# Kernel tuning notes

Measured on AMD Instinct MI355X. Metric: run time of the kernel, lower is better.

## Reference

```python
import jax, jax.numpy as jnp
import numpy as np

N = 50000          # num_entities
R = 16             # num_relations
D = 128            # embedding_dim
B = 4              # num_blocks
d = D // B         # block size (32)
E = 800000         # num edges


def setup_inputs() -> dict:
    key = jax.random.key(0)
    ks = jax.random.split(key, 9)
    s = 1.0 / np.sqrt(D)
    return {
        "edge_index": jax.random.randint(ks[0], (2, E), 0, N),
        "edge_type": jax.random.randint(ks[1], (E,), 0, R),
        "node_emb": jax.random.normal(ks[2], (N, D), jnp.float32) * s,
        "W1": jax.random.normal(ks[3], (R, B, d, d), jnp.float32) * s,
        "root1": jax.random.normal(ks[4], (D, D), jnp.float32) * s,
        "bias1": jax.random.normal(ks[5], (D,), jnp.float32) * 0.01,
        "W2": jax.random.normal(ks[6], (R, B, d, d), jnp.float32) * s,
        "root2": jax.random.normal(ks[7], (D, D), jnp.float32) * s,
        "bias2": jax.random.normal(ks[8], (D,), jnp.float32) * 0.01,
    }


def _rgcn_conv(x, src, dst, et, W, root, bias):
    # x: [N, D]; W: [R, B, d, d] block-diagonal per-relation weights.
    n = x.shape[0]
    # Transform every node under every relation (cheaper than gathering
    # per-edge weight blocks): [R, N, B, d] -> [R, N, D]
    allR = jnp.einsum('nbi,rbio->rnbo', x.reshape(n, B, d), W).reshape(R, n, D)
    msg = allR[et, src]                                   # [E, D] gather
    # Per-relation mean normalization 1/c_{i,r} (PyG RGCNConv aggr='mean'
    # applied per relation): count edges per (dst, relation) pair.
    seg = dst * R + et
    cnt = jax.ops.segment_sum(jnp.ones_like(et, x.dtype), seg, num_segments=n * R)
    norm = 1.0 / jnp.maximum(cnt[seg], 1.0)               # [E]
    agg = jax.ops.segment_sum(msg * norm[:, None], dst, num_segments=n)
    return agg + x @ root + bias


def reference(edge_index, edge_type, node_emb, W1, root1, bias1, W2, root2, bias2):
    src, dst = edge_index[0], edge_index[1]
    h = _rgcn_conv(node_emb, src, dst, edge_type, W1, root1, bias1)
    h = jax.nn.relu(h)  # dropout is identity in eval mode
    return _rgcn_conv(h, src, dst, edge_type, W2, root2, bias2)
```

## Files before the change

kernel.cpp:

```cpp
#include <hip/hip_runtime.h>
#include <hip/hip_bf16.h>

#define N_NODES 50000
#define N_REL   16
#define DIM     128
#define NBLK    4
#define BS      32
#define N_EDGES 800000
#define NSEG    (N_NODES * N_REL)
#define SCAN_BLK 1024
#define N_SCAN_BLKS ((NSEG + SCAN_BLK - 1) / SCAN_BLK)
#define NWT     (N_NODES / 16)

typedef __attribute__((ext_vector_type(8))) short s8v;
typedef __attribute__((ext_vector_type(8))) unsigned short u8v;
typedef __attribute__((ext_vector_type(4))) float f4v;

__device__ __forceinline__ float bf2f(unsigned short u) {
    return __uint_as_float(((unsigned int)u) << 16);
}
__device__ __forceinline__ unsigned short f2bfbits(float f) {
    unsigned int u = __float_as_uint(f);
    return (unsigned short)((u + 0x7fffu + ((u >> 16) & 1u)) >> 16);
}

__global__ __launch_bounds__(256) void count_kernel(const int* __restrict__ src,
                                                    const int* __restrict__ dst,
                                                    const int* __restrict__ et,
                                                    int* __restrict__ cnt,
                                                    int* __restrict__ used, int E) {
    int e = blockIdx.x * 256 + threadIdx.x;
    if (e < E) {
        int r = et[e];
        atomicAdd(&cnt[dst[e] * N_REL + r], 1);
        used[r * N_NODES + src[e]] = 1;
    }
}

__global__ __launch_bounds__(256) void scan1j_kernel(const int* __restrict__ cnt,
                                                     const int* __restrict__ used,
                                                     int* __restrict__ off,
                                                     int* __restrict__ cmap,
                                                     int2* __restrict__ bsum, int M) {
    const int t = threadIdx.x;
    const int base = blockIdx.x * SCAN_BLK + t * 4;
    int c[4], u[4];
#pragma unroll
    for (int i = 0; i < 4; ++i) {
        int idx = base + i;
        c[i] = (idx < M) ? cnt[idx] : 0;
        u[i] = (idx < M) ? used[idx] : 0;
    }
    int cs = c[0] + c[1] + c[2] + c[3];
    int us = u[0] + u[1] + u[2] + u[3];
    const int lane = t & 63, wid = t >> 6;
    int cinc = cs, uinc = us;
    for (int d = 1; d < 64; d <<= 1) {
        int a = __shfl_up(cinc, d, 64);
        int b = __shfl_up(uinc, d, 64);
        if (lane >= d) { cinc += a; uinc += b; }
    }
    __shared__ int cw[5], uw[5];
    if (lane == 63) { cw[wid] = cinc; uw[wid] = uinc; }
    __syncthreads();
    if (t == 0) {
        int a = 0, b = 0;
        for (int w = 0; w < 4; ++w) {
            int x = cw[w]; cw[w] = a; a += x;
            int y = uw[w]; uw[w] = b; b += y;
        }
        cw[4] = a; uw[4] = b;
    }
    __syncthreads();
    int cex = cinc - cs + cw[wid];
    int uex = uinc - us + uw[wid];
#pragma unroll
    for (int i = 0; i < 4; ++i) {
        int idx = base + i;
        if (idx < M) { off[idx] = cex; cmap[idx] = uex; }
        cex += c[i]; uex += u[i];
    }
    if (t == 0) bsum[blockIdx.x] = make_int2(cw[4], uw[4]);
}

__global__ __launch_bounds__(1024) void scan2j_kernel(int2* __restrict__ bsum, int nb) {
    const int t = threadIdx.x;
    int2 s = (t < nb) ? bsum[t] : make_int2(0, 0);
    const int lane = t & 63, wid = t >> 6;
    int ci = s.x, ui = s.y;
    for (int d = 1; d < 64; d <<= 1) {
        int a = __shfl_up(ci, d, 64);
        int b = __shfl_up(ui, d, 64);
        if (lane >= d) { ci += a; ui += b; }
    }
    __shared__ int cw[16], uw[16];
    if (lane == 63) { cw[wid] = ci; uw[wid] = ui; }
    __syncthreads();
    if (t == 0) {
        int a = 0, b = 0;
        for (int w = 0; w < 16; ++w) {
            int x = cw[w]; cw[w] = a; a += x;
            int y = uw[w]; uw[w] = b; b += y;
        }
    }
    __syncthreads();
    if (t < nb) bsum[t] = make_int2(ci - s.x + cw[wid], ui - s.y + uw[wid]);
}

__global__ __launch_bounds__(256) void scan3j_kernel(int* __restrict__ off,
                                                     int* __restrict__ cmap,
                                                     const int2* __restrict__ bsum, int M) {
    int i = blockIdx.x * 256 + threadIdx.x;
    if (i < M) {
        int2 b = bsum[i / SCAN_BLK];
        off[i] += b.x;
        cmap[i] += b.y;
    }
}

__global__ __launch_bounds__(256) void scatter_fast_kernel(const int* __restrict__ src,
                                                           const int* __restrict__ dst,
                                                           const int* __restrict__ et,
                                                           int* __restrict__ off,
                                                           const int* __restrict__ cnt,
                                                           const int* __restrict__ cmap,
                                                           int2* __restrict__ evec, int E) {
    int e = blockIdx.x * 256 + threadIdx.x;
    if (e < E) {
        int r = et[e];
        int seg = dst[e] * N_REL + r;
        int pos = atomicAdd(&off[seg], 1);
        float inv = 1.0f / (float)cnt[seg];
        int g = cmap[r * N_NODES + src[e]];
        evec[pos] = make_int2(g, __float_as_int(inv));
    }
}

__global__ __launch_bounds__(256) void scan1_kernel(const int* __restrict__ in,
                                                    int* __restrict__ out,
                                                    int* __restrict__ bsum, int M) {
    const int t = threadIdx.x;
    const int base = blockIdx.x * SCAN_BLK + t * 4;
    int v0 = (base + 0 < M) ? in[base + 0] : 0;
    int v1 = (base + 1 < M) ? in[base + 1] : 0;
    int v2 = (base + 2 < M) ? in[base + 2] : 0;
    int v3 = (base + 3 < M) ? in[base + 3] : 0;
    const int s = v0 + v1 + v2 + v3;
    const int lane = t & 63, wid = t >> 6;
    int inc = s;
    for (int d = 1; d < 64; d <<= 1) {
        int u = __shfl_up(inc, d, 64);
        if (lane >= d) inc += u;
    }
    __shared__ int wsum[5];
    if (lane == 63) wsum[wid] = inc;
    __syncthreads();
    if (t == 0) {
        int a = 0;
        for (int w = 0; w < 4; ++w) { int u = wsum[w]; wsum[w] = a; a += u; }
        wsum[4] = a;
    }
    __syncthreads();
    const int ex = inc - s + wsum[wid];
    if (base + 0 < M) out[base + 0] = ex;
    if (base + 1 < M) out[base + 1] = ex + v0;
    if (base + 2 < M) out[base + 2] = ex + v0 + v1;
    if (base + 3 < M) out[base + 3] = ex + v0 + v1 + v2;
    if (t == 0) bsum[blockIdx.x] = wsum[4];
}

__global__ __launch_bounds__(1024) void scan2_kernel(int* __restrict__ bsum, int nb) {
    const int t = threadIdx.x;
    int s = (t < nb) ? bsum[t] : 0;
    const int lane = t & 63, wid = t >> 6;
    int inc = s;
    for (int d = 1; d < 64; d <<= 1) {
        int u = __shfl_up(inc, d, 64);
        if (lane >= d) inc += u;
    }
    __shared__ int wsum[16];
    if (lane == 63) wsum[wid] = inc;
    __syncthreads();
    if (t == 0) {
        int a = 0;
        for (int w = 0; w < 16; ++w) { int u = wsum[w]; wsum[w] = a; a += u; }
    }
    __syncthreads();
    const int ex = inc - s + wsum[wid];
    if (t < nb) bsum[t] = ex;
}

__global__ __launch_bounds__(256) void scan3_kernel(int* __restrict__ out,
                                                    const int* __restrict__ bsum, int M) {
    int i = blockIdx.x * 256 + threadIdx.x;
    if (i < M) out[i] += bsum[i / SCAN_BLK];
}

__global__ __launch_bounds__(256) void scatter_old_kernel(const int* __restrict__ src,
                                                          const int* __restrict__ dst,
                                                          const int* __restrict__ et,
                                                          int* __restrict__ off,
                                                          int* __restrict__ srcs, int E) {
    int e = blockIdx.x * 256 + threadIdx.x;
    if (e < E) {
        int seg = dst[e] * N_REL + et[e];
        int pos = atomicAdd(&off[seg], 1);
        srcs[pos] = src[e];
    }
}

__global__ __launch_bounds__(256) void prep_kernel(const float* __restrict__ W1,
                                                   const float* __restrict__ W2,
                                                   const float* __restrict__ r1,
                                                   const float* __restrict__ r2,
                                                   ushort* __restrict__ WB1,
                                                   ushort* __restrict__ WB2,
                                                   ushort* __restrict__ RB1,
                                                   ushort* __restrict__ RB2) {
    int t = blockIdx.x * 256 + threadIdx.x;
    if (t < 262144) {
        const float* W = (t < 131072) ? W1 : W2;
        ushort* WB     = (t < 131072) ? WB1 : WB2;
        int idx = t & 131071;
        int i  = idx & 7;
        int lm = (idx >> 3) & 15;
        int kg = (idx >> 7) & 3;
        int mt = (idx >> 9) & 1;
        int b  = (idx >> 10) & 3;
        int r  = idx >> 12;
        WB[idx] = f2bfbits(W[((size_t)(r * 4 + b) * 32 + kg * 8 + i) * 32 + mt * 16 + lm]);
    } else if (t < 294912) {
        int u = t - 262144;
        const float* R = (u < 16384) ? r1 : r2;
        ushort* RB     = (u < 16384) ? RB1 : RB2;
        int idx = u & 16383;
        int i  = idx & 7;
        int lm = (idx >> 3) & 15;
        int kg = (idx >> 7) & 3;
        int kc = (idx >> 9) & 3;
        int mt = (idx >> 11) & 7;
        RB[idx] = f2bfbits(R[(size_t)(kc * 32 + kg * 8 + i) * DIM + mt * 16 + lm]);
    }
}

template<bool IN_BF16, bool OUT_BF16, bool RELU>
__global__ __launch_bounds__(256) void fused_kernel(const void* __restrict__ xin,
                                                    const ushort* __restrict__ WB,
                                                    const ushort* __restrict__ RB,
                                                    const float* __restrict__ bias,
                                                    const int* __restrict__ used,
                                                    const int* __restrict__ cmap,
                                                    char* __restrict__ tab,
                                                    float* __restrict__ scl,
                                                    void* __restrict__ outv) {
    const int wv = threadIdx.x >> 6;
    const int l  = threadIdx.x & 63;
    const int wt = blockIdx.x * 4 + wv;
    if (wt >= NWT) return;
    const int lm = l & 15;
    const int kg = l >> 4;
    const int node = wt * 16 + lm;
    const int y = blockIdx.y;

    s8v bfr[4];
#pragma unroll
    for (int b = 0; b < 4; ++b) {
        if (IN_BF16) {
            const ushort* xp = (const ushort*)xin + (size_t)node * DIM + b * BS + kg * 8;
            u8v u = *(const u8v*)xp;
#pragma unroll
            for (int i = 0; i < 8; ++i) {
                unsigned short us = u[i];
                if (RELU) us = (us & 0x8000u) ? (unsigned short)0 : us;
                bfr[b][i] = (short)us;
            }
        } else {
            const float* xp = (const float*)xin + (size_t)node * DIM + b * BS + kg * 8;
#pragma unroll
            for (int i = 0; i < 8; ++i) {
                float v = xp[i];
                if (RELU) v = fmaxf(v, 0.f);
                bfr[b][i] = (short)f2bfbits(v);
            }
        }
    }

    if (y < 4) {
        const int rbase = y * 4;
#pragma unroll 2
        for (int ri = 0; ri < 4; ++ri) {
            const int rr = rbase + ri;
            const int grow = rr * N_NODES + node;
            const int flag = used[grow];
            const int cid  = cmap[grow];
            f4v acc[4][2];
#pragma unroll
            for (int b = 0; b < 4; ++b) {
#pragma unroll
                for (int mt = 0; mt < 2; ++mt) {
                    s8v afrag = *(const s8v*)&WB[((((rr * 4 + b) * 2 + mt) * 4 + kg) * 16 + lm) * 8];
                    f4v z = {0.f, 0.f, 0.f, 0.f};
                    acc[b][mt] = __builtin_amdgcn_mfma_f32_16x16x32_bf16(afrag, bfr[b], z, 0, 0, 0);
                }
            }
            float t8[8];
#pragma unroll
            for (int b = 0; b < 4; ++b)
#pragma unroll
                for (int mt = 0; mt < 2; ++mt)
                    t8[b * 2 + mt] = fmaxf(fmaxf(fabsf(acc[b][mt][0]), fabsf(acc[b][mt][1])),
                                           fmaxf(fabsf(acc[b][mt][2]), fabsf(acc[b][mt][3])));
            float m = fmaxf(fmaxf(fmaxf(t8[0], t8[1]), fmaxf(t8[2], t8[3])),
                            fmaxf(fmaxf(t8[4], t8[5]), fmaxf(t8[6], t8[7])));
            m = fmaxf(m, __shfl_xor(m, 16, 64));
            m = fmaxf(m, __shfl_xor(m, 32, 64));
            m = fmaxf(m, 1e-30f);

            if (flag) {
                const float qs = 127.0f / m;
                unsigned int d[8];
#pragma unroll
                for (int b = 0; b < 4; ++b) {
#pragma unroll
                    for (int mt = 0; mt < 2; ++mt) {
                        int q0 = __float2int_rn(acc[b][mt][0] * qs);
                        int q1 = __float2int_rn(acc[b][mt][1] * qs);
                        int q2 = __float2int_rn(acc[b][mt][2] * qs);
                        int q3 = __float2int_rn(acc[b][mt][3] * qs);
                        unsigned int t01 = __builtin_amdgcn_perm((unsigned)q1, (unsigned)q0, 0x00000400u);
                        unsigned int t23 = __builtin_amdgcn_perm((unsigned)q3, (unsigned)q2, 0x00000400u);
                        d[b * 2 + mt] = __builtin_amdgcn_perm(t23, t01, 0x05040100u);
                    }
                }
                char* gp = tab + (size_t)cid * 128 + kg * 32;
                *(uint4*)gp        = make_uint4(d[0], d[1], d[2], d[3]);
                *(uint4*)(gp + 16) = make_uint4(d[4], d[5], d[6], d[7]);
                if (kg == 0) scl[cid] = m * (1.0f / 127.0f);
            }
        }
        return;
    }

#pragma unroll 2
    for (int mt = 0; mt < 8; ++mt) {
        const int col0 = mt * 16 + kg * 4;
        f4v acc = *(const f4v*)&bias[col0];
#pragma unroll
        for (int kc = 0; kc < 4; ++kc) {
            s8v afrag = *(const s8v*)&RB[(((mt * 4 + kc) * 4 + kg) * 16 + lm) * 8];
            acc = __builtin_amdgcn_mfma_f32_16x16x32_bf16(afrag, bfr[kc], acc, 0, 0, 0);
        }
        if (OUT_BF16) {
            unsigned int p0 = (unsigned int)f2bfbits(acc[0]) |
                              ((unsigned int)f2bfbits(acc[1]) << 16);
            unsigned int p1 = (unsigned int)f2bfbits(acc[2]) |
                              ((unsigned int)f2bfbits(acc[3]) << 16);
            *(uint2*)((ushort*)outv + (size_t)node * DIM + col0) = make_uint2(p0, p1);
        } else {
            *(f4v*)((float*)outv + (size_t)node * DIM + col0) = acc;
        }
    }
}

template<bool OUT_BF16>
__global__ __launch_bounds__(256) void agg8_kernel(const int2* __restrict__ evec,
                                                   const int* __restrict__ off,
                                                   const char* __restrict__ tab,
                                                   const float* __restrict__ scl,
                                                   void* __restrict__ outv) {
    const int hw = threadIdx.x >> 5;
    const int o  = threadIdx.x & 31;
    const int v  = blockIdx.x * 8 + hw;

    const int start = (v == 0) ? 0 : off[v * N_REL - 1];
    const int end   = off[v * N_REL + N_REL - 1];

    const int p = o >> 4;
    const int w = o & 15;

    float acc[8];
#pragma unroll
    for (int j = 0; j < 8; ++j) acc[j] = 0.f;

#pragma unroll 2
    for (int base = start; base < end; base += 4) {
        const int k0 = base + p;
        const int k1 = base + 2 + p;
        const int2 e0 = evec[min(k0, end - 1)];
        const int2 e1 = evec[min(k1, end - 1)];
        const int g0 = e0.x, g1 = e1.x;
        const float i0 = (k0 < end) ? __int_as_float(e0.y) : 0.f;
        const float i1 = (k1 < end) ? __int_as_float(e1.y) : 0.f;
        const uint2 q0 = *(const uint2*)(tab + (size_t)g0 * 128 + w * 8);
        const uint2 q1 = *(const uint2*)(tab + (size_t)g1 * 128 + w * 8);
        const float s0 = scl[g0] * i0;
        const float s1 = scl[g1] * i1;
#pragma unroll
        for (int j = 0; j < 4; ++j) {
            acc[j]     = fmaf((float)(int)(signed char)(q0.x >> (8 * j)), s0, acc[j]);
            acc[4 + j] = fmaf((float)(int)(signed char)(q0.y >> (8 * j)), s0, acc[4 + j]);
        }
#pragma unroll
        for (int j = 0; j < 4; ++j) {
            acc[j]     = fmaf((float)(int)(signed char)(q1.x >> (8 * j)), s1, acc[j]);
            acc[4 + j] = fmaf((float)(int)(signed char)(q1.y >> (8 * j)), s1, acc[4 + j]);
        }
    }
#pragma unroll
    for (int j = 0; j < 8; ++j)
        acc[j] += __shfl_xor(acc[j], 16, 32);

    if (o < 16) {
        const int base0 = (o & 3) * 32 + (o >> 2) * 4;
        if (OUT_BF16) {
            ushort* hp = (ushort*)outv + (size_t)v * DIM + base0;
            ushort4 a0 = *(ushort4*)hp;
            ushort4 a1 = *(ushort4*)(hp + 16);
            a0.x = f2bfbits(bf2f(a0.x) + acc[0]);
            a0.y = f2bfbits(bf2f(a0.y) + acc[1]);
            a0.z = f2bfbits(bf2f(a0.z) + acc[2]);
            a0.w = f2bfbits(bf2f(a0.w) + acc[3]);
            a1.x = f2bfbits(bf2f(a1.x) + acc[4]);
            a1.y = f2bfbits(bf2f(a1.y) + acc[5]);
            a1.z = f2bfbits(bf2f(a1.z) + acc[6]);
            a1.w = f2bfbits(bf2f(a1.w) + acc[7]);
            *(ushort4*)hp        = a0;
            *(ushort4*)(hp + 16) = a1;
        } else {
            float* op = (float*)outv + (size_t)v * DIM + base0;
            float4 r0 = *(float4*)op;
            float4 r1 = *(float4*)(op + 16);
            r0.x += acc[0]; r0.y += acc[1]; r0.z += acc[2]; r0.w += acc[3];
            r1.x += acc[4]; r1.y += acc[5]; r1.z += acc[6]; r1.w += acc[7];
            *(float4*)op        = r0;
            *(float4*)(op + 16) = r1;
        }
    }
}

template<bool RELU>
__global__ __launch_bounds__(256) void dense_old_kernel(const float* __restrict__ x,
                                                        const float* __restrict__ root,
                                                        const float* __restrict__ bias,
                                                        float* __restrict__ out) {
    const int wv = threadIdx.x >> 6;
    const int l  = threadIdx.x & 63;
    const int wt = blockIdx.x * 4 + wv;
    if (wt >= NWT) return;
    const int nbase = wt * 16;
    const int lm = l & 15;
    const int kg = l >> 4;
    const int node = nbase + lm;

    s8v bfr[4];
#pragma unroll
    for (int kc = 0; kc < 4; ++kc) {
        const float* xp = &x[(size_t)node * DIM + kc * BS + kg * 8];
#pragma unroll
        for (int i = 0; i < 8; ++i) {
            float v = xp[i];
            if (RELU) v = fmaxf(v, 0.f);
            bfr[kc][i] = (short)f2bfbits(v);
        }
    }
#pragma unroll 2
    for (int mt = 0; mt < 8; ++mt) {
        const int col0 = mt * 16 + kg * 4;
        f4v acc = *(const f4v*)&bias[col0];
#pragma unroll
        for (int kc = 0; kc < 4; ++kc) {
            const float* rp = &root[(size_t)(kc * BS + kg * 8) * DIM + mt * 16 + lm];
            s8v afrag;
#pragma unroll
            for (int i = 0; i < 8; ++i)
                afrag[i] = (short)f2bfbits(rp[i * DIM]);
            acc = __builtin_amdgcn_mfma_f32_16x16x32_bf16(afrag, bfr[kc], acc, 0, 0, 0);
        }
        *(f4v*)&out[(size_t)node * DIM + col0] = acc;
    }
}

template<bool RELU>
__global__ __launch_bounds__(256) void agg_fallback_kernel(const int* __restrict__ srcs,
                                                           const int* __restrict__ off,
                                                           const int* __restrict__ cnt,
                                                           const float* __restrict__ x,
                                                           const float* __restrict__ W,
                                                           float* __restrict__ out) {
    __shared__ float Wsh[N_REL * BS * BS];
    const int bblk = blockIdx.y;
    for (int idx = threadIdx.x * 4; idx < N_REL * BS * BS; idx += 1024) {
        int r = idx >> 10, rest = idx & 1023;
        *(float4*)&Wsh[idx] = *(const float4*)&W[(r * NBLK + bblk) * 1024 + rest];
    }
    __syncthreads();
    const int hw = threadIdx.x >> 5;
    const int o  = threadIdx.x & 31;
    const int v  = blockIdx.x * 8 + hw;
    int endv = 0, cv = 0;
    if (o < N_REL) { endv = off[v * N_REL + o]; cv = cnt[v * N_REL + o]; }
    float acc = out[v * DIM + bblk * BS + o];
    for (int r = 0; r < N_REL; ++r) {
        const int c = __shfl(cv, r, 32);
        if (c == 0) continue;
        const int end = __shfl(endv, r, 32);
        float xs = 0.f;
        for (int k = end - c; k < end; ++k) {
            const int s = srcs[k];
            float xv = x[s * DIM + bblk * BS + o];
            if (RELU) xv = fmaxf(xv, 0.f);
            xs += xv;
        }
        xs *= (1.0f / (float)c);
        const float* wr = &Wsh[r * (BS * BS)];
#pragma unroll
        for (int i = 0; i < BS; i += 2) {
            float xi0 = __shfl(xs, i, 32);
            float xi1 = __shfl(xs, i + 1, 32);
            acc = fmaf(xi0, wr[i * BS + o], acc);
            acc = fmaf(xi1, wr[(i + 1) * BS + o], acc);
        }
    }
    out[v * DIM + bblk * BS + o] = acc;
}

extern "C" void kernel_launch(void* const* d_in, const int* in_sizes, int n_in,
                              void* d_out, int out_size, void* d_ws, size_t ws_size,
                              hipStream_t stream) {
    const int*   edge_index = (const int*)d_in[0];
    const int*   src   = edge_index;
    const int*   dstv  = edge_index + N_EDGES;
    const int*   et    = (const int*)d_in[1];
    const float* x0    = (const float*)d_in[2];
    const float* W1    = (const float*)d_in[3];
    const float* root1 = (const float*)d_in[4];
    const float* bias1 = (const float*)d_in[5];
    const float* W2    = (const float*)d_in[6];
    const float* root2 = (const float*)d_in[7];
    const float* bias2 = (const float*)d_in[8];
    float* out = (float*)d_out;

    char* ws = (char*)d_ws;
    ushort* h    = (ushort*)ws;
    int*    cnt  = (int*)   (ws + 12800000);
    int*    used = (int*)   (ws + 16000000);
    int*    off  = (int*)   (ws + 19200000);
    int*    cmap = (int*)   (ws + 22400000);
    int2*   evec = (int2*)  (ws + 25600000);
    int2*   bsum = (int2*)  (ws + 32000000);
    ushort* WB1  = (ushort*)(ws + 32008192);
    ushort* WB2  = (ushort*)(ws + 32270336);
    ushort* RB1  = (ushort*)(ws + 32532480);
    ushort* RB2  = (ushort*)(ws + 32565248);
    float*  scl  = (float*) (ws + 32598016);
    char*   tab  =          (ws + 35798016);
    const size_t FAST_NEED = 138198016ull;

    const int egrid = (N_EDGES + 255) / 256;
    const int tgrid = (NWT + 3) / 4;

    if (ws_size >= FAST_NEED) {
        prep_kernel<<<1152, 256, 0, stream>>>(W1, W2, root1, root2, WB1, WB2, RB1, RB2);
        hipMemsetAsync(cnt, 0, 2 * (size_t)NSEG * sizeof(int), stream);
        count_kernel<<<egrid, 256, 0, stream>>>(src, dstv, et, cnt, used, N_EDGES);
        scan1j_kernel<<<N_SCAN_BLKS, 256, 0, stream>>>(cnt, used, off, cmap, bsum, NSEG);
        scan2j_kernel<<<1, 1024, 0, stream>>>(bsum, N_SCAN_BLKS);
        scan3j_kernel<<<(NSEG + 255) / 256, 256, 0, stream>>>(off, cmap, bsum, NSEG);
        scatter_fast_kernel<<<egrid, 256, 0, stream>>>(src, dstv, et, off, cnt, cmap,
                                                       evec, N_EDGES);

        dim3 fgrid(tgrid, 5);
        const int ngrid = N_NODES / 8;

        fused_kernel<false, true, false><<<fgrid, 256, 0, stream>>>(
            x0, WB1, RB1, bias1, used, cmap, tab, scl, h);
        agg8_kernel<true><<<ngrid, 256, 0, stream>>>(evec, off, tab, scl, h);

        fused_kernel<true, false, true><<<fgrid, 256, 0, stream>>>(
            h, WB2, RB2, bias2, used, cmap, tab, scl, out);
        agg8_kernel<false><<<ngrid, 256, 0, stream>>>(evec, off, tab, scl, out);
    } else {
        float* hf    = (float*)d_ws;
        int*   cntf  = (int*)((char*)d_ws + 25600000);
        int*   offf  = (int*)((char*)d_ws + 28800000);
        int*   srcsf = (int*)((char*)d_ws + 32000000);
        int*   bsumf = (int*)((char*)d_ws + 35200000);
        int*   usedD = offf;

        hipMemsetAsync(cntf, 0, (size_t)NSEG * sizeof(int), stream);
        count_kernel<<<egrid, 256, 0, stream>>>(src, dstv, et, cntf, usedD, N_EDGES);
        scan1_kernel<<<N_SCAN_BLKS, 256, 0, stream>>>(cntf, offf, bsumf, NSEG);
        scan2_kernel<<<1, 1024, 0, stream>>>(bsumf, N_SCAN_BLKS);
        scan3_kernel<<<(NSEG + 255) / 256, 256, 0, stream>>>(offf, bsumf, NSEG);
        scatter_old_kernel<<<egrid, 256, 0, stream>>>(src, dstv, et, offf, srcsf, N_EDGES);

        dim3 fgrid2(N_NODES / 8, NBLK);
        dense_old_kernel<false><<<tgrid, 256, 0, stream>>>(x0, root1, bias1, hf);
        agg_fallback_kernel<false><<<fgrid2, 256, 0, stream>>>(srcsf, offf, cntf, x0, W1, hf);
        dense_old_kernel<true><<<tgrid, 256, 0, stream>>>(hf, root2, bias2, out);
        agg_fallback_kernel<true><<<fgrid2, 256, 0, stream>>>(srcsf, offf, cntf, hf, W2, out);
    }
}
```

Measured before the change: 255.7 us.

## Fold scan block offsets into consumers and regroup fused kernel relations

Drops the third scan pass that added per-block prefix sums into the offset and compaction arrays. Each consumer (scatter, fused transform, aggregation) now adds the block sum itself when it reads. Separately, the fused kernel grid shrinks from 5 y-slices to 2: each slice handles 8 relations, and slice 0 also computes the root/bias dense part. This saves one kernel launch and a full pass over 800k entries, at the cost of extra bsum loads and less parallelism in the fused kernel.

After: 244.6 us. 1.05x faster.

```diff
diff --git a/kernel.cpp b/kernel.cpp
--- a/kernel.cpp
+++ b/kernel.cpp
@@ -107,31 +107,22 @@
     if (t < nb) bsum[t] = make_int2(ci - s.x + cw[wid], ui - s.y + uw[wid]);
 }
 
-__global__ __launch_bounds__(256) void scan3j_kernel(int* __restrict__ off,
-                                                     int* __restrict__ cmap,
-                                                     const int2* __restrict__ bsum, int M) {
-    int i = blockIdx.x * 256 + threadIdx.x;
-    if (i < M) {
-        int2 b = bsum[i / SCAN_BLK];
-        off[i] += b.x;
-        cmap[i] += b.y;
-    }
-}
-
 __global__ __launch_bounds__(256) void scatter_fast_kernel(const int* __restrict__ src,
                                                            const int* __restrict__ dst,
                                                            const int* __restrict__ et,
                                                            int* __restrict__ off,
                                                            const int* __restrict__ cnt,
                                                            const int* __restrict__ cmap,
+                                                           const int2* __restrict__ bsum,
                                                            int2* __restrict__ evec, int E) {
     int e = blockIdx.x * 256 + threadIdx.x;
     if (e < E) {
         int r = et[e];
         int seg = dst[e] * N_REL + r;
-        int pos = atomicAdd(&off[seg], 1);
+        int pos = atomicAdd(&off[seg], 1) + bsum[seg >> 10].x;
         float inv = 1.0f / (float)cnt[seg];
-        int g = cmap[r * N_NODES + src[e]];
+        int grow = r * N_NODES + src[e];
+        int g = cmap[grow] + bsum[grow >> 10].y;
         evec[pos] = make_int2(g, __float_as_int(inv));
     }
 }
@@ -250,6 +241,7 @@
                                                     const float* __restrict__ bias,
                                                     const int* __restrict__ used,
                                                     const int* __restrict__ cmap,
+                                                    const int2* __restrict__ bsum,
                                                     char* __restrict__ tab,
                                                     float* __restrict__ scl,
                                                     void* __restrict__ outv) {
@@ -257,10 +249,10 @@
     const int l  = threadIdx.x & 63;
     const int wt = blockIdx.x * 4 + wv;
     if (wt >= NWT) return;
+    const int rbase = blockIdx.y * 8;
     const int lm = l & 15;
     const int kg = l >> 4;
     const int node = wt * 16 + lm;
-    const int y = blockIdx.y;
 
     s8v bfr[4];
 #pragma unroll
@@ -285,79 +277,77 @@
         }
     }
 
-    if (y < 4) {
-        const int rbase = y * 4;
 #pragma unroll 2
-        for (int ri = 0; ri < 4; ++ri) {
-            const int rr = rbase + ri;
-            const int grow = rr * N_NODES + node;
-            const int flag = used[grow];
-            const int cid  = cmap[grow];
-            f4v acc[4][2];
+    for (int ri = 0; ri < 8; ++ri) {
+        const int rr = rbase + ri;
+        const int grow = rr * N_NODES + node;
+        const int flag = used[grow];
+        const int cid  = cmap[grow] + bsum[grow >> 10].y;
+        f4v acc[4][2];
+#pragma unroll
+        for (int b = 0; b < 4; ++b) {
+#pragma unroll
+            for (int mt = 0; mt < 2; ++mt) {
+                s8v afrag = *(const s8v*)&WB[((((rr * 4 + b) * 2 + mt) * 4 + kg) * 16 + lm) * 8];
+                f4v z = {0.f, 0.f, 0.f, 0.f};
+                acc[b][mt] = __builtin_amdgcn_mfma_f32_16x16x32_bf16(afrag, bfr[b], z, 0, 0, 0);
+            }
+        }
+        float t8[8];
+#pragma unroll
+        for (int b = 0; b < 4; ++b)
+#pragma unroll
+            for (int mt = 0; mt < 2; ++mt)
+                t8[b * 2 + mt] = fmaxf(fmaxf(fabsf(acc[b][mt][0]), fabsf(acc[b][mt][1])),
+                                       fmaxf(fabsf(acc[b][mt][2]), fabsf(acc[b][mt][3])));
+        float m = fmaxf(fmaxf(fmaxf(t8[0], t8[1]), fmaxf(t8[2], t8[3])),
+                        fmaxf(fmaxf(t8[4], t8[5]), fmaxf(t8[6], t8[7])));
+        m = fmaxf(m, __shfl_xor(m, 16, 64));
+        m = fmaxf(m, __shfl_xor(m, 32, 64));
+        m = fmaxf(m, 1e-30f);
+
+        if (flag) {
+            const float qs = 127.0f / m;
+            unsigned int d[8];
 #pragma unroll
             for (int b = 0; b < 4; ++b) {
 #pragma unroll
                 for (int mt = 0; mt < 2; ++mt) {
-                    s8v afrag = *(const s8v*)&WB[((((rr * 4 + b) * 2 + mt) * 4 + kg) * 16 + lm) * 8];
-                    f4v z = {0.f, 0.f, 0.f, 0.f};
-                    acc[b][mt] = __builtin_amdgcn_mfma_f32_16x16x32_bf16(afrag, bfr[b], z, 0, 0, 0);
+                    int q0 = __float2int_rn(acc[b][mt][0] * qs);
+                    int q1 = __float2int_rn(acc[b][mt][1] * qs);
+                    int q2 = __float2int_rn(acc[b][mt][2] * qs);
+                    int q3 = __float2int_rn(acc[b][mt][3] * qs);
+                    unsigned int t01 = __builtin_amdgcn_perm((unsigned)q1, (unsigned)q0, 0x00000400u);
+                    unsigned int t23 = __builtin_amdgcn_perm((unsigned)q3, (unsigned)q2, 0x00000400u);
+                    d[b * 2 + mt] = __builtin_amdgcn_perm(t23, t01, 0x05040100u);
                 }
             }
-            float t8[8];
-#pragma unroll
-            for (int b = 0; b < 4; ++b)
-#pragma unroll
-                for (int mt = 0; mt < 2; ++mt)
-                    t8[b * 2 + mt] = fmaxf(fmaxf(fabsf(acc[b][mt][0]), fabsf(acc[b][mt][1])),
-                                           fmaxf(fabsf(acc[b][mt][2]), fabsf(acc[b][mt][3])));
-            float m = fmaxf(fmaxf(fmaxf(t8[0], t8[1]), fmaxf(t8[2], t8[3])),
-                            fmaxf(fmaxf(t8[4], t8[5]), fmaxf(t8[6], t8[7])));
-            m = fmaxf(m, __shfl_xor(m, 16, 64));
-            m = fmaxf(m, __shfl_xor(m, 32, 64));
-            m = fmaxf(m, 1e-30f);
-
-            if (flag) {
-                const float qs = 127.0f / m;
-                unsigned int d[8];
-#pragma unroll
-                for (int b = 0; b < 4; ++b) {
-#pragma unroll
-                    for (int mt = 0; mt < 2; ++mt) {
-                        int q0 = __float2int_rn(acc[b][mt][0] * qs);
-                        int q1 = __float2int_rn(acc[b][mt][1] * qs);
-                        int q2 = __float2int_rn(acc[b][mt][2] * qs);
-                        int q3 = __float2int_rn(acc[b][mt][3] * qs);
-                        unsigned int t01 = __builtin_amdgcn_perm((unsigned)q1, (unsigned)q0, 0x00000400u);
-                        unsigned int t23 = __builtin_amdgcn_perm((unsigned)q3, (unsigned)q2, 0x00000400u);
-                        d[b * 2 + mt] = __builtin_amdgcn_perm(t23, t01, 0x05040100u);
-                    }
-                }
-                char* gp = tab + (size_t)cid * 128 + kg * 32;
-                *(uint4*)gp        = make_uint4(d[0], d[1], d[2], d[3]);
-                *(uint4*)(gp + 16) = make_uint4(d[4], d[5], d[6], d[7]);
-                if (kg == 0) scl[cid] = m * (1.0f / 127.0f);
+            char* gp = tab + (size_t)cid * 128 + kg * 32;
+            *(uint4*)gp        = make_uint4(d[0], d[1], d[2], d[3]);
+            *(uint4*)(gp + 16) = make_uint4(d[4], d[5], d[6], d[7]);
+            if (kg == 0) scl[cid] = m * (1.0f / 127.0f);
+        }
+    }
+
+    if (blockIdx.y == 0) {
+#pragma unroll 2
+        for (int mt = 0; mt < 8; ++mt) {
+            const int col0 = mt * 16 + kg * 4;
+            f4v acc = *(const f4v*)&bias[col0];
+#pragma unroll
+            for (int kc = 0; kc < 4; ++kc) {
+                s8v afrag = *(const s8v*)&RB[(((mt * 4 + kc) * 4 + kg) * 16 + lm) * 8];
+                acc = __builtin_amdgcn_mfma_f32_16x16x32_bf16(afrag, bfr[kc], acc, 0, 0, 0);
             }
-        }
-        return;
-    }
-
-#pragma unroll 2
-    for (int mt = 0; mt < 8; ++mt) {
-        const int col0 = mt * 16 + kg * 4;
-        f4v acc = *(const f4v*)&bias[col0];
-#pragma unroll
-        for (int kc = 0; kc < 4; ++kc) {
-            s8v afrag = *(const s8v*)&RB[(((mt * 4 + kc) * 4 + kg) * 16 + lm) * 8];
-            acc = __builtin_amdgcn_mfma_f32_16x16x32_bf16(afrag, bfr[kc], acc, 0, 0, 0);
-        }
-        if (OUT_BF16) {
-            unsigned int p0 = (unsigned int)f2bfbits(acc[0]) |
-                              ((unsigned int)f2bfbits(acc[1]) << 16);
-            unsigned int p1 = (unsigned int)f2bfbits(acc[2]) |
-                              ((unsigned int)f2bfbits(acc[3]) << 16);
-            *(uint2*)((ushort*)outv + (size_t)node * DIM + col0) = make_uint2(p0, p1);
-        } else {
-            *(f4v*)((float*)outv + (size_t)node * DIM + col0) = acc;
+            if (OUT_BF16) {
+                unsigned int p0 = (unsigned int)f2bfbits(acc[0]) |
+                                  ((unsigned int)f2bfbits(acc[1]) << 16);
+                unsigned int p1 = (unsigned int)f2bfbits(acc[2]) |
+                                  ((unsigned int)f2bfbits(acc[3]) << 16);
+                *(uint2*)((ushort*)outv + (size_t)node * DIM + col0) = make_uint2(p0, p1);
+            } else {
+                *(f4v*)((float*)outv + (size_t)node * DIM + col0) = acc;
+            }
         }
     }
 }
@@ -365,6 +355,7 @@
 template<bool OUT_BF16>
 __global__ __launch_bounds__(256) void agg8_kernel(const int2* __restrict__ evec,
                                                    const int* __restrict__ off,
+                                                   const int2* __restrict__ bsum,
                                                    const char* __restrict__ tab,
                                                    const float* __restrict__ scl,
                                                    void* __restrict__ outv) {
@@ -372,8 +363,13 @@
     const int o  = threadIdx.x & 31;
     const int v  = blockIdx.x * 8 + hw;
 
-    const int start = (v == 0) ? 0 : off[v * N_REL - 1];
-    const int end   = off[v * N_REL + N_REL - 1];
+    const int ei = v * N_REL + N_REL - 1;
+    const int end = off[ei] + bsum[ei >> 10].x;
+    int start = 0;
+    if (v > 0) {
+        const int si = v * N_REL - 1;
+        start = off[si] + bsum[si >> 10].x;
+    }
 
     const int p = o >> 4;
     const int w = o & 15;
@@ -565,20 +561,19 @@
         count_kernel<<<egrid, 256, 0, stream>>>(src, dstv, et, cnt, used, N_EDGES);
         scan1j_kernel<<<N_SCAN_BLKS, 256, 0, stream>>>(cnt, used, off, cmap, bsum, NSEG);
         scan2j_kernel<<<1, 1024, 0, stream>>>(bsum, N_SCAN_BLKS);
-        scan3j_kernel<<<(NSEG + 255) / 256, 256, 0, stream>>>(off, cmap, bsum, NSEG);
         scatter_fast_kernel<<<egrid, 256, 0, stream>>>(src, dstv, et, off, cnt, cmap,
-                                                       evec, N_EDGES);
-
-        dim3 fgrid(tgrid, 5);
+                                                       bsum, evec, N_EDGES);
+
+        dim3 fgrid(tgrid, 2);
         const int ngrid = N_NODES / 8;
 
         fused_kernel<false, true, false><<<fgrid, 256, 0, stream>>>(
-            x0, WB1, RB1, bias1, used, cmap, tab, scl, h);
-        agg8_kernel<true><<<ngrid, 256, 0, stream>>>(evec, off, tab, scl, h);
+            x0, WB1, RB1, bias1, used, cmap, bsum, tab, scl, h);
+        agg8_kernel<true><<<ngrid, 256, 0, stream>>>(evec, off, bsum, tab, scl, h);
 
         fused_kernel<true, false, true><<<fgrid, 256, 0, stream>>>(
-            h, WB2, RB2, bias2, used, cmap, tab, scl, out);
-        agg8_kernel<false><<<ngrid, 256, 0, stream>>>(evec, off, tab, scl, out);
+            h, WB2, RB2, bias2, used, cmap, bsum, tab, scl, out);
+        agg8_kernel<false><<<ngrid, 256, 0, stream>>>(evec, off, bsum, tab, scl, out);
     } else {
         float* hf    = (float*)d_ws;
         int*   cntf  = (int*)((char*)d_ws + 25600000);
```
